# Optimization experiments

Hardware: AMD Instinct MI355X
Metric: run time of the kernel (lower is better)

The kernel has to match this reference:

```python
import jax, jax.numpy as jnp
import numpy as np

N_SRC = 100000
N_DST = 100000
E = 1600000
D_IN = 128
D_REL = 128
K = 8        # num_heads
D_OUT = 16   # out_dim per head; K*D_OUT = 128
SLOPE = 0.2  # LeakyReLU negative slope


def setup_inputs() -> dict:
    key = jax.random.key(0)
    ks = jax.random.split(key, 11)
    s = 0.05  # weight init scale
    return {
        "feat_src": jax.random.normal(ks[0], (N_SRC, D_IN), jnp.float32),
        "feat_dst": jax.random.normal(ks[1], (N_DST, D_IN), jnp.float32),
        "feat_rel": jax.random.normal(ks[2], (D_REL,), jnp.float32),
        "W_src": jax.random.normal(ks[3], (D_IN, K * D_OUT), jnp.float32) * s,
        "b_src": jnp.zeros((K * D_OUT,), jnp.float32),
        "W_dst": jax.random.normal(ks[4], (D_IN, K * D_OUT), jnp.float32) * s,
        "b_dst": jnp.zeros((K * D_OUT,), jnp.float32),
        "W_rel": jax.random.normal(ks[5], (D_REL, 2 * K * D_OUT), jnp.float32) * s,
        "b_rel": jnp.zeros((2 * K * D_OUT,), jnp.float32),
        "src_idx": jax.random.randint(ks[6], (E,), 0, N_SRC, dtype=jnp.int32),
        "dst_idx": jax.random.randint(ks[7], (E,), 0, N_DST, dtype=jnp.int32),
    }


def reference(feat_src, feat_dst, feat_rel, W_src, b_src, W_dst, b_dst,
              W_rel, b_rel, src_idx, dst_idx):
    # Linear projections (feat_drop = 0 -> identity)
    fs = (feat_src @ W_src + b_src).reshape(-1, K, D_OUT)   # (N_src, K, D)
    fd = (feat_dst @ W_dst + b_dst).reshape(-1, K, D_OUT)   # (N_dst, K, D)
    attn = (feat_rel @ W_rel + b_rel).reshape(K, 2 * D_OUT)  # (K, 2D)

    el = jnp.einsum('nkd,kd->nk', fs, attn[:, :D_OUT])  # (N_src, K)
    er = jnp.einsum('nkd,kd->nk', fd, attn[:, D_OUT:])  # (N_dst, K)

    # Per-edge scores: u_add_v then LeakyReLU
    e = el[src_idx] + er[dst_idx]                        # (E, K)
    e = jnp.where(e >= 0, e, SLOPE * e)

    # edge_softmax: softmax over incoming edges per destination node
    emax = jax.ops.segment_max(e, dst_idx, num_segments=N_DST)  # (N_dst, K)
    a = jnp.exp(e - emax[dst_idx])                               # (E, K)
    asum = jax.ops.segment_sum(a, dst_idx, num_segments=N_DST)   # (N_dst, K)
    a = a / asum[dst_idx]

    # u_mul_e + sum aggregation
    msg = fs[src_idx] * a[:, :, None]                            # (E, K, D)
    out = jax.ops.segment_sum(msg, dst_idx, num_segments=N_DST)  # (N_dst, K, D)
    return out.reshape(N_DST, K * D_OUT)
```

## Files before the change

kernel.cpp:

```cpp
#include <hip/hip_runtime.h>
#include <hip/hip_fp16.h>
#include <hip/hip_bf16.h>

#define SLOPE 0.2f
#define EPB 4096
#define LDA 136
#define CAPLG 12

typedef short bf16x8 __attribute__((ext_vector_type(8)));
typedef float f32x4 __attribute__((ext_vector_type(4)));

__device__ __forceinline__ unsigned short f2bf(float x) {
    unsigned u = __float_as_uint(x);
    u += 0x7FFFu + ((u >> 16) & 1u);
    return (unsigned short)(u >> 16);
}

__global__ void prep_kernel(const float* __restrict__ feat_rel,
                            const float* __restrict__ W_rel,
                            const float* __restrict__ b_rel,
                            float* __restrict__ attn,
                            const float* __restrict__ W_src,
                            unsigned short* __restrict__ WtS,
                            const float* __restrict__ W_dst,
                            unsigned short* __restrict__ WtD,
                            int* __restrict__ bcur) {
    int bx = blockIdx.x;
    if (bx < 128) {
        const float* W = (bx < 64) ? W_src : W_dst;
        unsigned short* Wt = (bx < 64) ? WtS : WtD;
        int t = (bx & 63) * 256 + threadIdx.x;
        int n = t >> 7, k = t & 127;
        Wt[n * 128 + k] = f2bf(W[k * 128 + n]);
    } else if (bx == 128) {
        int j = threadIdx.x;
        float acc = b_rel[j];
        for (int d = 0; d < 128; ++d)
            acc = fmaf(feat_rel[d], W_rel[d * 256 + j], acc);
        attn[j] = acc;
    } else {
#pragma unroll
        for (int i = 0; i < 4; ++i) {
            int j = threadIdx.x + i * 256;
            bcur[j] = j << CAPLG;
        }
    }
}

#define SMEM_BYTES ((64 * LDA + 128 * LDA) * 2 + 128 * 4)

__global__ __launch_bounds__(256) void gemm_part_kernel(
    const float* __restrict__ featS, const unsigned short* __restrict__ WtS,
    const float* __restrict__ bS,
    const float* __restrict__ featD, const unsigned short* __restrict__ WtD,
    const float* __restrict__ bD,
    const float* __restrict__ attn, __half* __restrict__ fs,
    float* __restrict__ el, float* __restrict__ er,
    int Ms, int Md, int nbs, int ngemm,
    const int* __restrict__ src_idx, const int* __restrict__ dst_idx,
    int* __restrict__ bcur, int* __restrict__ part, int ne)
{
    __shared__ __align__(16) unsigned char smem[SMEM_BYTES];

    int bx = blockIdx.x;
    int t = threadIdx.x;

    if (bx >= ngemm) {
        int* hist = (int*)smem;
        int* base = hist + 1024;
        for (int i = t; i < 1024; i += 256) hist[i] = 0;
        int e0 = (bx - ngemm) * EPB;
        int myS[16], myD[16];
        __syncthreads();
#pragma unroll
        for (int i = 0; i < 16; ++i) {
            int e = e0 + i * 256 + t;
            if (e < ne) {
                myS[i] = src_idx[e];
                myD[i] = dst_idx[e];
                atomicAdd(&hist[myD[i] >> 7], 1);
            } else myD[i] = -1;
        }
        __syncthreads();
        for (int b = t; b < 1024; b += 256) {
            int c = hist[b];
            if (c > 0) {
                base[b] = atomicAdd(&bcur[b], c);
                hist[b] = 0;
            }
        }
        __syncthreads();
#pragma unroll
        for (int i = 0; i < 16; ++i) {
            if (myD[i] >= 0) {
                int b = myD[i] >> 7;
                int slot = base[b] + atomicAdd(&hist[b], 1);
                part[slot] = myS[i] | ((myD[i] & 127) << 20);
            }
        }
        return;
    }

    unsigned short* sA = (unsigned short*)smem;
    unsigned short* sB = sA + 64 * LDA;
    float* sAtt = (float*)(smem + (64 * LDA + 128 * LDA) * 2);

    const float* feat; const unsigned short* Wt; const float* bias;
    __half* f_out; float* e_out; int attn_off, M, row0;
    if (bx < nbs) {
        feat = featS; Wt = WtS; bias = bS; f_out = fs; e_out = el;
        attn_off = 0; M = Ms; row0 = bx * 64;
    } else {
        feat = featD; Wt = WtD; bias = bD; f_out = nullptr; e_out = er;
        attn_off = 16; M = Md; row0 = (bx - nbs) * 64;
    }

    if (t < 128) sAtt[t] = attn[(t >> 4) * 32 + attn_off + (t & 15)];

#pragma unroll
    for (int i = 0; i < 8; ++i) {
        int idx = t + i * 256;
        int row = idx >> 5, k4 = idx & 31;
        int grow = row0 + row;
        float4 v = {0.f, 0.f, 0.f, 0.f};
        if (grow < M) v = *(const float4*)(feat + (size_t)grow * 128 + k4 * 4);
        ushort4 b;
        b.x = f2bf(v.x); b.y = f2bf(v.y); b.z = f2bf(v.z); b.w = f2bf(v.w);
        *(ushort4*)&sA[row * LDA + k4 * 4] = b;
    }
#pragma unroll
    for (int i = 0; i < 8; ++i) {
        int idx = t + i * 256;
        int n = idx >> 4, koff = (idx & 15) * 8;
        *(uint4*)&sB[n * LDA + koff] = *(const uint4*)&Wt[n * 128 + koff];
    }
    __syncthreads();

    int wv = t >> 6, lane = t & 63;
    int m = lane & 15, quad = lane >> 4;
    int n0 = wv * 32;

    f32x4 acc[2][4];
#pragma unroll
    for (int ct = 0; ct < 2; ++ct)
#pragma unroll
        for (int rt = 0; rt < 4; ++rt) acc[ct][rt] = (f32x4){0.f, 0.f, 0.f, 0.f};

#pragma unroll
    for (int ks = 0; ks < 4; ++ks) {
        bf16x8 a[4], b[2];
#pragma unroll
        for (int rt = 0; rt < 4; ++rt)
            a[rt] = *(const bf16x8*)&sA[(rt * 16 + m) * LDA + ks * 32 + quad * 8];
#pragma unroll
        for (int ct = 0; ct < 2; ++ct)
            b[ct] = *(const bf16x8*)&sB[(n0 + ct * 16 + m) * LDA + ks * 32 + quad * 8];
#pragma unroll
        for (int ct = 0; ct < 2; ++ct)
#pragma unroll
            for (int rt = 0; rt < 4; ++rt)
                acc[ct][rt] = __builtin_amdgcn_mfma_f32_16x16x32_bf16(
                    a[rt], b[ct], acc[ct][rt], 0, 0, 0);
    }

    __syncthreads();
    __half* sF = (__half*)sA;
#pragma unroll
    for (int ct = 0; ct < 2; ++ct) {
        int col = n0 + ct * 16 + m;
        float bias_v = bias[col];
#pragma unroll
        for (int rt = 0; rt < 4; ++rt) {
            f32x4 c = acc[ct][rt];
#pragma unroll
            for (int r = 0; r < 4; ++r)
                sF[(rt * 16 + quad * 4 + r) * LDA + col] = __float2half(c[r] + bias_v);
        }
    }
    __syncthreads();

    int mrem = M - row0;

    if (f_out) {
#pragma unroll
        for (int i = 0; i < 4; ++i) {
            int idx = t + i * 256;
            int row = idx >> 4, c8 = (idx & 15) * 8;
            if (row < mrem) {
                uint4 v = *(const uint4*)&sF[row * LDA + c8];
                *(uint4*)(f_out + (size_t)(row0 + row) * 128 + c8) = v;
            }
        }
    }
#pragma unroll
    for (int i = 0; i < 2; ++i) {
        int p = t + i * 256;
        int row = p >> 3, h = p & 7;
        if (row < mrem) {
            const __half* fp = &sF[row * LDA + h * 16];
            const float* ap = &sAtt[h * 16];
            float acc2 = 0.f;
#pragma unroll
            for (int j = 0; j < 16; ++j)
                acc2 = fmaf((float)fp[j], ap[j], acc2);
            e_out[(size_t)(row0 + row) * 8 + h] = acc2;
        }
    }
}

__global__ __launch_bounds__(256) void place_kernel(
    const int* __restrict__ part, const int* __restrict__ bcur,
    int* __restrict__ csr, int* __restrict__ roff, int* __restrict__ deg,
    int n_dst)
{
    int b = blockIdx.x;
    int node0 = b << 7;
    int tid = threadIdx.x;
    __shared__ int cnt[128];
    __shared__ int off[128];
    if (tid < 128) cnt[tid] = 0;
    int pstart = b << CAPLG;
    int pend = bcur[b];
    __syncthreads();

    for (int pi = pstart + tid; pi < pend; pi += 256)
        atomicAdd(&cnt[part[pi] >> 20], 1);
    __syncthreads();

    if (tid < 128) off[tid] = cnt[tid];
    __syncthreads();
    for (int o = 1; o < 128; o <<= 1) {
        int x = 0;
        if (tid < 128 && tid >= o) x = off[tid - o];
        __syncthreads();
        if (tid < 128) off[tid] += x;
        __syncthreads();
    }
    if (tid < 128) {
        int excl = off[tid] - cnt[tid];
        off[tid] = excl;
        int node = node0 + tid;
        if (node < n_dst) {
            roff[node] = pstart + excl;
            deg[node]  = cnt[tid];
        }
        cnt[tid] = 0;
    }
    __syncthreads();

    for (int pi = pstart + tid; pi < pend; pi += 256) {
        int val = part[pi];
        int dl = val >> 20;
        int fine = atomicAdd(&cnt[dl], 1);
        csr[pstart + off[dl] + fine] = val & 0xFFFFF;
    }
}

__global__ __launch_bounds__(256) void agg_kernel(
    const __half* __restrict__ fs, const float* __restrict__ el,
    const float* __restrict__ er, const int* __restrict__ roff,
    const int* __restrict__ deg, const int* __restrict__ csr,
    float* __restrict__ out, int n)
{
    int lane = threadIdx.x & 63;
    int wv = threadIdx.x >> 6;
    int g = lane >> 4;
    int q = lane & 15;
    int h = q >> 1;
    int node = blockIdx.x * 16 + wv * 4 + g;
    bool alive = node < n;
    int start = 0, d = 0;
    float er8 = 0.f;
    if (alive) {
        start = roff[node];
        d = deg[node];
        er8 = er[(size_t)node * 8 + h];
    }

    float acc[8] = {0.f, 0.f, 0.f, 0.f, 0.f, 0.f, 0.f, 0.f};
    float wsum = 0.f;
    int i = 0;
    for (; i + 4 <= d; i += 4) {
        int s[4]; float ex[4]; uint4 v[4];
#pragma unroll
        for (int j = 0; j < 4; ++j)
            s[j] = __builtin_nontemporal_load(csr + start + i + j);
#pragma unroll
        for (int j = 0; j < 4; ++j)
            ex[j] = el[(size_t)s[j] * 8 + h];
#pragma unroll
        for (int j = 0; j < 4; ++j)
            v[j] = *(const uint4*)(fs + (size_t)s[j] * 128 + q * 8);
#pragma unroll
        for (int j = 0; j < 4; ++j) {
            float x = ex[j] + er8;
            x = (x < 0.f) ? SLOPE * x : x;
            float w = __expf(x);
            const __half* hp = (const __half*)&v[j];
#pragma unroll
            for (int k = 0; k < 8; ++k)
                acc[k] = fmaf(w, (float)hp[k], acc[k]);
            wsum += w;
        }
    }
    for (; i < d; ++i) {
        int s0 = __builtin_nontemporal_load(csr + start + i);
        float x = el[(size_t)s0 * 8 + h] + er8;
        x = (x < 0.f) ? SLOPE * x : x;
        float w0 = __expf(x);
        uint4 v0 = *(const uint4*)(fs + (size_t)s0 * 128 + q * 8);
        const __half* hp = (const __half*)&v0;
#pragma unroll
        for (int k = 0; k < 8; ++k)
            acc[k] = fmaf(w0, (float)hp[k], acc[k]);
        wsum += w0;
    }
    if (alive) {
        float inv = (d > 0) ? 1.0f / wsum : 0.f;
        f32x4 o0 = {acc[0] * inv, acc[1] * inv, acc[2] * inv, acc[3] * inv};
        f32x4 o1 = {acc[4] * inv, acc[5] * inv, acc[6] * inv, acc[7] * inv};
        __builtin_nontemporal_store(o0, (f32x4*)(out + (size_t)node * 128 + q * 8));
        __builtin_nontemporal_store(o1, (f32x4*)(out + (size_t)node * 128 + q * 8 + 4));
    }
}

extern "C" void kernel_launch(void* const* d_in, const int* in_sizes, int n_in,
                              void* d_out, int out_size, void* d_ws, size_t ws_size,
                              hipStream_t stream) {
    const float* feat_src = (const float*)d_in[0];
    const float* feat_dst = (const float*)d_in[1];
    const float* feat_rel = (const float*)d_in[2];
    const float* W_src    = (const float*)d_in[3];
    const float* b_src    = (const float*)d_in[4];
    const float* W_dst    = (const float*)d_in[5];
    const float* b_dst    = (const float*)d_in[6];
    const float* W_rel    = (const float*)d_in[7];
    const float* b_rel    = (const float*)d_in[8];
    const int*   src_idx  = (const int*)d_in[9];
    const int*   dst_idx  = (const int*)d_in[10];
    float* out = (float*)d_out;

    int n_src = in_sizes[0] / 128;
    int n_dst = in_sizes[1] / 128;
    int ne    = in_sizes[9];
    int nbuck = (n_dst + 127) >> 7;
    size_t slab = (size_t)nbuck << CAPLG;

    char* w = (char*)d_ws;
    auto alloc = [&](size_t b) { char* p = w; w += (b + 255) & ~(size_t)255; return p; };
    __half* fs   = (__half*)alloc((size_t)n_src * 128 * 2);
    float*  el   = (float*)alloc((size_t)n_src * 8 * 4);
    float*  er   = (float*)alloc((size_t)n_dst * 8 * 4);
    float*  attn = (float*)alloc(256 * 4);
    unsigned short* WtS = (unsigned short*)alloc(128 * 128 * 2);
    unsigned short* WtD = (unsigned short*)alloc(128 * 128 * 2);
    int*    deg  = (int*)alloc((size_t)n_dst * 4);
    int*    roff = (int*)alloc((size_t)n_dst * 4);
    int*    bcur = (int*)alloc(1024 * 4);
    int*    csr  = (int*)alloc(slab * 4);
    int*    part = (int*)alloc(slab * 4);

    prep_kernel<<<130, 256, 0, stream>>>(
        feat_rel, W_rel, b_rel, attn, W_src, WtS, W_dst, WtD, bcur);

    int nbs = (n_src + 63) / 64, nbd = (n_dst + 63) / 64;
    int ngemm = nbs + nbd;
    int nparts = (ne + EPB - 1) / EPB;
    gemm_part_kernel<<<ngemm + nparts, 256, 0, stream>>>(
        feat_src, WtS, b_src, feat_dst, WtD, b_dst, attn,
        fs, el, er, n_src, n_dst, nbs, ngemm,
        src_idx, dst_idx, bcur, part, ne);

    place_kernel<<<nbuck, 256, 0, stream>>>(part, bcur, csr, roff, deg, n_dst);

    agg_kernel<<<(n_dst + 15) / 16, 256, 0, stream>>>(
        fs, el, er, roff, deg, csr, out, n_dst);
}
```

Baseline: 292.9 us.

## Fuse CSR placement into aggregation using per-block shared-memory bucket sorting

```diff
diff --git a/kernel.cpp b/kernel.cpp
--- a/kernel.cpp
+++ b/kernel.cpp
@@ -6,6 +6,7 @@
 #define EPB 4096
 #define LDA 136
 #define CAPLG 12
+#define SCAP 1024
 
 typedef short bf16x8 __attribute__((ext_vector_type(8)));
 typedef float f32x4 __attribute__((ext_vector_type(4)));
@@ -208,72 +209,63 @@
     }
 }
 
-__global__ __launch_bounds__(256) void place_kernel(
-    const int* __restrict__ part, const int* __restrict__ bcur,
-    int* __restrict__ csr, int* __restrict__ roff, int* __restrict__ deg,
-    int n_dst)
+__global__ __launch_bounds__(256) void bucket_agg_kernel(
+    const __half* __restrict__ fs, const float* __restrict__ el,
+    const float* __restrict__ er, const int* __restrict__ part,
+    const int* __restrict__ bcur, float* __restrict__ out,
+    int n_dst, int nbuck, int NB8)
 {
-    int b = blockIdx.x;
-    int node0 = b << 7;
+    __shared__ int csr_l[SCAP];
+    __shared__ int cnt[16];
+    __shared__ int off16[16];
+    __shared__ int cur[16];
+
+    int b = blockIdx.x % NB8;
+    int s = blockIdx.x / NB8;
+    if (b >= nbuck) return;
+    int node0 = (b << 7) + (s << 4);
+    if (node0 >= n_dst) return;
+
     int tid = threadIdx.x;
-    __shared__ int cnt[128];
-    __shared__ int off[128];
-    if (tid < 128) cnt[tid] = 0;
+    if (tid < 16) { cnt[tid] = 0; cur[tid] = 0; }
     int pstart = b << CAPLG;
     int pend = bcur[b];
     __syncthreads();
 
-    for (int pi = pstart + tid; pi < pend; pi += 256)
-        atomicAdd(&cnt[part[pi] >> 20], 1);
-    __syncthreads();
-
-    if (tid < 128) off[tid] = cnt[tid];
-    __syncthreads();
-    for (int o = 1; o < 128; o <<= 1) {
-        int x = 0;
-        if (tid < 128 && tid >= o) x = off[tid - o];
-        __syncthreads();
-        if (tid < 128) off[tid] += x;
-        __syncthreads();
-    }
-    if (tid < 128) {
-        int excl = off[tid] - cnt[tid];
-        off[tid] = excl;
-        int node = node0 + tid;
-        if (node < n_dst) {
-            roff[node] = pstart + excl;
-            deg[node]  = cnt[tid];
-        }
-        cnt[tid] = 0;
-    }
-    __syncthreads();
-
+    for (int pi = pstart + tid; pi < pend; pi += 256) {
+        int dl = part[pi] >> 20;
+        if ((dl >> 4) == s) atomicAdd(&cnt[dl & 15], 1);
+    }
+    __syncthreads();
+    if (tid == 0) {
+        int r = 0;
+#pragma unroll
+        for (int i = 0; i < 16; ++i) { off16[i] = r; r += cnt[i]; }
+    }
+    __syncthreads();
     for (int pi = pstart + tid; pi < pend; pi += 256) {
         int val = part[pi];
         int dl = val >> 20;
-        int fine = atomicAdd(&cnt[dl], 1);
-        csr[pstart + off[dl] + fine] = val & 0xFFFFF;
-    }
-}
-
-__global__ __launch_bounds__(256) void agg_kernel(
-    const __half* __restrict__ fs, const float* __restrict__ el,
-    const float* __restrict__ er, const int* __restrict__ roff,
-    const int* __restrict__ deg, const int* __restrict__ csr,
-    float* __restrict__ out, int n)
-{
-    int lane = threadIdx.x & 63;
-    int wv = threadIdx.x >> 6;
+        if ((dl >> 4) == s) {
+            int f = atomicAdd(&cur[dl & 15], 1);
+            csr_l[off16[dl & 15] + f] = val & 0xFFFFF;
+        }
+    }
+    __syncthreads();
+
+    int lane = tid & 63;
+    int wv = tid >> 6;
     int g = lane >> 4;
     int q = lane & 15;
     int h = q >> 1;
-    int node = blockIdx.x * 16 + wv * 4 + g;
-    bool alive = node < n;
+    int nl = wv * 4 + g;
+    int node = node0 + nl;
+    bool alive = node < n_dst;
     int start = 0, d = 0;
     float er8 = 0.f;
     if (alive) {
-        start = roff[node];
-        d = deg[node];
+        start = off16[nl];
+        d = cnt[nl];
         er8 = er[(size_t)node * 8 + h];
     }
 
@@ -281,16 +273,16 @@
     float wsum = 0.f;
     int i = 0;
     for (; i + 4 <= d; i += 4) {
-        int s[4]; float ex[4]; uint4 v[4];
+        int sj[4]; float ex[4]; uint4 v[4];
 #pragma unroll
         for (int j = 0; j < 4; ++j)
-            s[j] = __builtin_nontemporal_load(csr + start + i + j);
+            sj[j] = csr_l[start + i + j];
 #pragma unroll
         for (int j = 0; j < 4; ++j)
-            ex[j] = el[(size_t)s[j] * 8 + h];
+            ex[j] = el[(size_t)sj[j] * 8 + h];
 #pragma unroll
         for (int j = 0; j < 4; ++j)
-            v[j] = *(const uint4*)(fs + (size_t)s[j] * 128 + q * 8);
+            v[j] = *(const uint4*)(fs + (size_t)sj[j] * 128 + q * 8);
 #pragma unroll
         for (int j = 0; j < 4; ++j) {
             float x = ex[j] + er8;
@@ -304,7 +296,7 @@
         }
     }
     for (; i < d; ++i) {
-        int s0 = __builtin_nontemporal_load(csr + start + i);
+        int s0 = csr_l[start + i];
         float x = el[(size_t)s0 * 8 + h] + er8;
         x = (x < 0.f) ? SLOPE * x : x;
         float w0 = __expf(x);
@@ -344,6 +336,7 @@
     int n_dst = in_sizes[1] / 128;
     int ne    = in_sizes[9];
     int nbuck = (n_dst + 127) >> 7;
+    int NB8   = (nbuck + 7) & ~7;
     size_t slab = (size_t)nbuck << CAPLG;
 
     char* w = (char*)d_ws;
@@ -354,10 +347,7 @@
     float*  attn = (float*)alloc(256 * 4);
     unsigned short* WtS = (unsigned short*)alloc(128 * 128 * 2);
     unsigned short* WtD = (unsigned short*)alloc(128 * 128 * 2);
-    int*    deg  = (int*)alloc((size_t)n_dst * 4);
-    int*    roff = (int*)alloc((size_t)n_dst * 4);
     int*    bcur = (int*)alloc(1024 * 4);
-    int*    csr  = (int*)alloc(slab * 4);
     int*    part = (int*)alloc(slab * 4);
 
     prep_kernel<<<130, 256, 0, stream>>>(
@@ -371,8 +361,6 @@
         fs, el, er, n_src, n_dst, nbs, ngemm,
         src_idx, dst_idx, bcur, part, ne);
 
-    place_kernel<<<nbuck, 256, 0, stream>>>(part, bcur, csr, roff, deg, n_dst);
-
-    agg_kernel<<<(n_dst + 15) / 16, 256, 0, stream>>>(
-        fs, el, er, roff, deg, csr, out, n_dst);
-}
+    bucket_agg_kernel<<<NB8 * 8, 256, 0, stream>>>(
+        fs, el, er, part, bcur, out, n_dst, nbuck, NB8);
+}
```

New measurement: 283.4 us. 1.03x faster.
